# Optimization experiments

Measured on AMD Instinct MI355X. Metric: run time of the kernel, lower is better.

Reference implementation:

```python
import jax, jax.numpy as jnp
import numpy as np

DIM = 2048
N_HEADS = 32
N_KV_HEADS = 8
HEAD_DIM = DIM // N_HEADS  # 64
N_REP = N_HEADS // N_KV_HEADS  # 4
B, S = 2, 2048
MASK_VAL = -32768.0


def setup_inputs() -> dict:
    key = jax.random.key(0)
    ks = jax.random.split(key, 7)
    x = jax.random.normal(ks[0], (B, S, DIM), dtype=jnp.float32)
    freqs_cos = jax.random.uniform(ks[1], (S, HEAD_DIM // 2), dtype=jnp.float32)
    freqs_sin = jax.random.uniform(ks[2], (S, HEAD_DIM // 2), dtype=jnp.float32)
    sc = 1.0 / np.sqrt(DIM)
    wq = jax.random.normal(ks[3], (N_HEADS * HEAD_DIM, DIM), dtype=jnp.float32) * sc
    wk = jax.random.normal(ks[4], (N_KV_HEADS * HEAD_DIM, DIM), dtype=jnp.float32) * sc
    wv = jax.random.normal(ks[5], (N_KV_HEADS * HEAD_DIM, DIM), dtype=jnp.float32) * sc
    wo = jax.random.normal(ks[6], (DIM, N_HEADS * HEAD_DIM), dtype=jnp.float32) * sc
    return {"x": x, "freqs_cos": freqs_cos, "freqs_sin": freqs_sin,
            "wq": wq, "wk": wk, "wv": wv, "wo": wo}


def _apply_rope(q, k, cos, sin):
    # q: [B,S,H,D], k: [B,S,Hkv,D]; interleaved real/imag pairs in last dim
    def rot(t):
        tr = t.reshape(t.shape[:-1] + (-1, 2))  # [..., D/2, 2]
        t_r, t_i = tr[..., 0], tr[..., 1]
        c = cos[None, :, None, :]  # broadcast over batch and heads
        s = sin[None, :, None, :]
        o_r = t_r * c - t_i * s
        o_i = t_r * s + t_i * c
        return jnp.stack([o_r, o_i], axis=-1).reshape(t.shape)
    return rot(q), rot(k)


def reference(x, freqs_cos, freqs_sin, wq, wk, wv, wo):
    bsz, seqlen, _ = x.shape
    xq = (x @ wq.T).reshape(bsz, seqlen, N_HEADS, HEAD_DIM)
    xk = (x @ wk.T).reshape(bsz, seqlen, N_KV_HEADS, HEAD_DIM)
    xv = (x @ wv.T).reshape(bsz, seqlen, N_KV_HEADS, HEAD_DIM)
    xq, xk = _apply_rope(xq, xk, freqs_cos, freqs_sin)
    # GQA: repeat each kv head n_rep times contiguously (matches per-head cat loop)
    xk = jnp.repeat(xk, N_REP, axis=2)  # [B,S,H,D]
    xv = jnp.repeat(xv, N_REP, axis=2)
    # [B,H,S,D]
    q = xq.transpose(0, 2, 1, 3)
    k = xk.transpose(0, 2, 1, 3)
    v = xv.transpose(0, 2, 1, 3)
    scores = jnp.einsum('bhqd,bhkd->bhqk', q, k) / jnp.sqrt(jnp.float32(HEAD_DIM))
    causal = jnp.triu(jnp.full((seqlen, seqlen), MASK_VAL, dtype=scores.dtype), k=1)
    scores = scores + causal[None, None, :, :]
    probs = jax.nn.softmax(scores.astype(jnp.float32), axis=-1).astype(q.dtype)
    out = jnp.einsum('bhqk,bhkd->bhqd', probs, v)
    out = out.transpose(0, 2, 1, 3).reshape(bsz, seqlen, -1)
    return out @ wo.T
```

## Files before the change

### kernel.cpp

```cpp
#include <hip/hip_runtime.h>
#include <hip/hip_bf16.h>
#include <type_traits>

typedef __bf16 bf16;
typedef __bf16 bf16x2 __attribute__((ext_vector_type(2)));
typedef __bf16 bf16x4 __attribute__((ext_vector_type(4)));
typedef __bf16 bf16x8 __attribute__((ext_vector_type(8)));
typedef float f32x4 __attribute__((ext_vector_type(4)));

#define AS1 __attribute__((address_space(1)))
#define AS3 __attribute__((address_space(3)))

#define KAPPA 0.180336880111f

__device__ __forceinline__ void load_lds16(const void* g, void* l) {
  __builtin_amdgcn_global_load_lds((AS1 void*)g, (AS3 void*)l, 16, 0, 0);
}
__device__ __forceinline__ float exp2_fast(float x) {
  return __builtin_amdgcn_exp2f(x);
}

__global__ void f2b_all(const float* __restrict__ x, const float* __restrict__ wq,
                        const float* __restrict__ wk, const float* __restrict__ wv,
                        const float* __restrict__ wo, bf16* __restrict__ xb,
                        bf16* __restrict__ wqkv, bf16* __restrict__ wob) {
  int bid = blockIdx.x;
  if (bid < 8192) {
    int i = (bid * 256 + threadIdx.x) * 4;
    float4 v = *(const float4*)(x + i);
    bf16x4 o = {(bf16)v.x, (bf16)v.y, (bf16)v.z, (bf16)v.w};
    *(bf16x4*)(xb + i) = o;
    return;
  }
  int bid2 = bid - 8192;
  const float* src;
  bf16* dst;
  int nblk, kblk, nb;
  if (bid2 < 3072) {
    nblk = bid2 >> 6;
    kblk = bid2 & 63;
    int n0 = nblk * 64;
    if (n0 < 2048) { src = wq; nb = n0; }
    else if (n0 < 2560) { src = wk; nb = n0 - 2048; }
    else { src = wv; nb = n0 - 2560; }
    dst = wqkv;
  } else {
    int bid3 = bid2 - 3072;
    nblk = bid3 >> 6;
    kblk = bid3 & 63;
    src = wo;
    nb = nblk * 64;
    dst = wob;
  }
  const int t = threadIdx.x, j = t >> 6, l = t & 63;
  const int n = nb + j * 16 + (l & 15);
  const int k = kblk * 32 + (l >> 4) * 8;
  float4 v0 = *(const float4*)(src + (size_t)n * 2048 + k);
  float4 v1 = *(const float4*)(src + (size_t)n * 2048 + k + 4);
  bf16x8 o = {(bf16)v0.x, (bf16)v0.y, (bf16)v0.z, (bf16)v0.w,
              (bf16)v1.x, (bf16)v1.y, (bf16)v1.z, (bf16)v1.w};
  *(bf16x8*)((char*)dst + ((size_t)(nblk * 64 + kblk)) * 4096 + j * 1024 +
             l * 16) = o;
}

__global__ __launch_bounds__(256, 3) void gemm_qkv(const bf16* __restrict__ A,
                                                   const bf16* __restrict__ Bw,
                                                   const float* __restrict__ fc,
                                                   const float* __restrict__ fs,
                                                   bf16* __restrict__ Qro,
                                                   bf16* __restrict__ Kro,
                                                   bf16* __restrict__ Vt) {
  const int K = 2048;
  __shared__ bf16 As[3][128][32];
  const int t = threadIdx.x;
  const int wave = t >> 6, lane = t & 63, qd = lane >> 4, ln = lane & 15;
  const int wm = (wave >> 1) * 64;
  const int wn = (wave & 1) * 64;
  const int bn = blockIdx.x;
  const size_t bm = (size_t)blockIdx.y * 128;

  const bf16* Ab = A + bm * (size_t)K;
  const int n0 = bn * 2 + (wn >> 6);
  const char* Bb = (const char*)Bw + (size_t)n0 * 262144 + (size_t)lane * 16;

  auto stage = [&](int tk, int slot) {
#pragma unroll
    for (int sub = 0; sub < 2; sub++) {
      int e = sub * 256 + t;
      int ro = e >> 2, gs = (e & 3) ^ ((ro >> 1) & 3);
      load_lds16(Ab + (size_t)ro * K + tk * 32 + gs * 8,
                 (char*)As + slot * 8192 + sub * 4096 + wave * 1024);
    }
  };

  f32x4 acc[4][4] = {};
  const int segoff = (qd ^ ((ln >> 1) & 3)) << 4;
  bf16x8 b0[4], b1[4];

#pragma unroll
  for (int j = 0; j < 4; j++)
    b0[j] = *(const bf16x8*)(Bb + (size_t)j * 1024);
  stage(0, 0);
  stage(1, 1);
  asm volatile("s_waitcnt vmcnt(2)" ::: "memory");
  __builtin_amdgcn_s_barrier();

  auto step = [&](int tk, bf16x8 (&cb)[4], bf16x8 (&nb)[4]) {
    if (tk < 62) stage(tk + 2, (tk + 2) % 3);
    if (tk < 63) {
#pragma unroll
      for (int j = 0; j < 4; j++)
        nb[j] = *(const bf16x8*)(Bb + (size_t)(tk + 1) * 4096 + j * 1024);
    }
    const char* Asl = (const char*)As + (tk % 3) * 8192;
    bf16x8 af[4];
#pragma unroll
    for (int i = 0; i < 4; i++)
      af[i] = *(const bf16x8*)(Asl + (wm + i * 16 + ln) * 64 + segoff);
    if (tk <= 61) asm volatile("s_waitcnt lgkmcnt(0) vmcnt(6)" ::: "memory");
    else if (tk == 62) asm volatile("s_waitcnt lgkmcnt(0) vmcnt(4)" ::: "memory");
    else asm volatile("s_waitcnt lgkmcnt(0) vmcnt(0)" ::: "memory");
    __builtin_amdgcn_sched_barrier(0);
    __builtin_amdgcn_s_setprio(1);
#pragma unroll
    for (int i = 0; i < 4; i++)
#pragma unroll
      for (int j = 0; j < 4; j++)
        acc[i][j] = __builtin_amdgcn_mfma_f32_16x16x32_bf16(af[i], cb[j],
                                                            acc[i][j], 0, 0, 0);
    __builtin_amdgcn_s_setprio(0);
    if (tk < 63) __builtin_amdgcn_s_barrier();
  };

  for (int tk = 0; tk < 64; tk += 2) {
    step(tk, b0, b1);
    step(tk + 1, b1, b0);
  }

  const int b = (int)(bm >> 11);
  const int sb = (int)(bm & 2047) + wm;
  const bool odd = ln & 1;

  if (bn < 20) {
    const bool isQ = bn < 16;
    const float kap = isQ ? KAPPA : 1.0f;
    const int hh = isQ ? (bn * 2 + (wn >> 6)) : ((bn - 16) * 2 + (wn >> 6));
    bf16* dst = isQ ? (Qro + ((size_t)(b * 32 + hh) * 2048) * 64)
                    : (Kro + ((size_t)(b * 8 + hh) * 2048) * 64);
#pragma unroll
    for (int i = 0; i < 4; i++) {
#pragma unroll
      for (int j = 0; j < 4; j++) {
        const int d = j * 16 + ln;
        const int i_f = d >> 1;
#pragma unroll
        for (int r = 0; r < 4; r++) {
          int s = sb + i * 16 + qd * 4 + r;
          float v = acc[i][j][r];
          float p = __shfl_xor(v, 1);
          float cv = fc[s * 32 + i_f] * kap;
          float sv = fs[s * 32 + i_f] * kap;
          float o = odd ? (p * sv + v * cv) : (v * cv - p * sv);
          dst[(size_t)s * 64 + d] = (bf16)o;
        }
      }
    }
  } else {
    const int kh = (bn - 20) * 2 + (wn >> 6);
#pragma unroll
    for (int i = 0; i < 4; i++)
#pragma unroll
      for (int j = 0; j < 4; j++) {
        const int d = j * 16 + ln;
        int s = sb + i * 16 + qd * 4;
        bf16x4 ov = {(bf16)acc[i][j][0], (bf16)acc[i][j][1],
                     (bf16)acc[i][j][2], (bf16)acc[i][j][3]};
        *(bf16x4*)&Vt[((size_t)(b * 8 + kh) * 64 + d) * 2048 + s] = ov;
      }
  }
}

__global__ __launch_bounds__(256, 4) void gemm_bt(const bf16* __restrict__ A,
                                                  const bf16* __restrict__ Bw,
                                                  float* __restrict__ C) {
  const int K = 2048, N = 2048;
  __shared__ bf16 As[3][64][32];
  const int t = threadIdx.x;
  const int wave = t >> 6, lane = t & 63, qd = lane >> 4, ln = lane & 15;
  const int wm = (wave >> 1) * 32;
  const int wn = (wave & 1) * 64;
  const size_t bm = (size_t)blockIdx.y * 64;
  const size_t bn = (size_t)blockIdx.x * 128;

  const bf16* Ab = A + bm * (size_t)K;
  const int n0 = (int)(bn >> 6) + (wn >> 6);
  const char* Bb = (const char*)Bw + (size_t)n0 * 262144 + (size_t)lane * 16;

  auto stage = [&](int tk, int slot) {
    int ro = t >> 2, gs = (t & 3) ^ ((ro >> 1) & 3);
    load_lds16(Ab + (size_t)ro * K + tk * 32 + gs * 8,
               (char*)As + slot * 4096 + wave * 1024);
  };

  f32x4 acc[2][4] = {};
  const int segoff = (qd ^ ((ln >> 1) & 3)) << 4;
  bf16x8 b0[4], b1[4];

#pragma unroll
  for (int j = 0; j < 4; j++)
    b0[j] = *(const bf16x8*)(Bb + (size_t)j * 1024);
  stage(0, 0);
  stage(1, 1);
  asm volatile("s_waitcnt vmcnt(1)" ::: "memory");
  __builtin_amdgcn_s_barrier();

  auto step = [&](int tk, bf16x8 (&cb)[4], bf16x8 (&nb)[4]) {
    if (tk < 62) stage(tk + 2, (tk + 2) % 3);
    if (tk < 63) {
#pragma unroll
      for (int j = 0; j < 4; j++)
        nb[j] = *(const bf16x8*)(Bb + (size_t)(tk + 1) * 4096 + j * 1024);
    }
    const char* Asl = (const char*)As + (tk % 3) * 4096;
    bf16x8 af[2];
#pragma unroll
    for (int i = 0; i < 2; i++)
      af[i] = *(const bf16x8*)(Asl + (wm + i * 16 + ln) * 64 + segoff);
    if (tk <= 61) asm volatile("s_waitcnt lgkmcnt(0) vmcnt(5)" ::: "memory");
    else if (tk == 62) asm volatile("s_waitcnt lgkmcnt(0) vmcnt(4)" ::: "memory");
    else asm volatile("s_waitcnt lgkmcnt(0) vmcnt(0)" ::: "memory");
    __builtin_amdgcn_sched_barrier(0);
    __builtin_amdgcn_s_setprio(1);
#pragma unroll
    for (int i = 0; i < 2; i++)
#pragma unroll
      for (int j = 0; j < 4; j++)
        acc[i][j] = __builtin_amdgcn_mfma_f32_16x16x32_bf16(af[i], cb[j],
                                                            acc[i][j], 0, 0, 0);
    __builtin_amdgcn_s_setprio(0);
    if (tk < 63) __builtin_amdgcn_s_barrier();
  };

  for (int tk = 0; tk < 64; tk += 2) {
    step(tk, b0, b1);
    step(tk + 1, b1, b0);
  }

#pragma unroll
  for (int i = 0; i < 2; i++)
#pragma unroll
    for (int j = 0; j < 4; j++)
#pragma unroll
      for (int r = 0; r < 4; r++) {
        size_t row = bm + wm + i * 16 + qd * 4 + r;
        size_t col = bn + wn + j * 16 + ln;
        C[row * N + col] = acc[i][j][r];
      }
}

__global__ __launch_bounds__(256, 3) void attn_fwd(const bf16* __restrict__ Q,
                                                   const bf16* __restrict__ Kg,
                                                   const bf16* __restrict__ Vg,
                                                   bf16* __restrict__ O) {
  __shared__ bf16 Ks[2][64][64];
  __shared__ bf16 Vs[2][64][64];
  __shared__ bf16 Ps[128][64];
  const int t = threadIdx.x;
  const int wave = t >> 6, lane = t & 63, qd = lane >> 4, ln = lane & 15;
  const int bid = blockIdx.x;
  const int qt = 15 - (bid >> 6);
  const int bh = bid & 63;
  const int b = bh >> 5, h = bh & 31, kh = h >> 2;
  const bf16* Qb = Q + ((size_t)(b * 32 + h) * 2048 + qt * 128) * 64;
  const bf16* Kb = Kg + (size_t)(b * 8 + kh) * 2048 * 64;
  const bf16* Vb = Vg + (size_t)(b * 8 + kh) * 64 * 2048;
  char* PsB = (char*)Ps;

  bf16x8 qf[2][2];
#pragma unroll
  for (int kk = 0; kk < 2; kk++)
#pragma unroll
    for (int mi = 0; mi < 2; mi++)
      qf[kk][mi] = *(const bf16x8*)(Qb + (wave * 32 + mi * 16 + ln) * 64 +
                                    (kk * 4 + qd) * 8);

  auto stageKV = [&](int kb, int buf) {
#pragma unroll
    for (int i = 0; i < 2; i++) {
      int e = i * 256 + t;
      int row = e >> 3, sg = (e & 7) ^ (row & 7);
      load_lds16(Kb + (size_t)(kb * 64 + row) * 64 + sg * 8,
                 (char*)Ks + buf * 8192 + i * 4096 + wave * 1024);
      load_lds16(Vb + (size_t)row * 2048 + kb * 64 + sg * 8,
                 (char*)Vs + buf * 8192 + i * 4096 + wave * 1024);
    }
  };

  f32x4 o_acc[4][2] = {};
  float l_st[2] = {0.f, 0.f};
  const int q0 = qt * 128 + wave * 32;
  const int nkb = 2 * qt + 2;

  stageKV(0, 0);
  __syncthreads();

  for (int kb = 0; kb < nkb; kb++) {
    const int cur = kb & 1;
    if (kb + 1 < nkb) stageKV(kb + 1, cur ^ 1);
    const char* Ksl = (const char*)Ks + cur * 8192;
    const char* Vsl = (const char*)Vs + cur * 8192;

    f32x4 s_acc[4][2] = {};
#pragma unroll
    for (int kk = 0; kk < 2; kk++) {
      bf16x8 ak[4];
#pragma unroll
      for (int j = 0; j < 4; j++) {
        int row = j * 16 + ln;
        int ph = (kk * 4 + qd) ^ (ln & 7);
        ak[j] = *(const bf16x8*)(Ksl + row * 128 + ph * 16);
      }
#pragma unroll
      for (int j = 0; j < 4; j++)
#pragma unroll
        for (int mi = 0; mi < 2; mi++)
          s_acc[j][mi] = __builtin_amdgcn_mfma_f32_16x16x32_bf16(
              ak[j], qf[kk][mi], s_acc[j][mi], 0, 0, 0);
    }

    auto smax = [&](auto maskc) {
      constexpr bool MASK = decltype(maskc)::value;
#pragma unroll
      for (int mi = 0; mi < 2; mi++) {
        const int qv = q0 + mi * 16 + ln;
        const int prow = wave * 32 + mi * 16 + ln;
        float rs = 0.f;
#pragma unroll
        for (int j = 0; j < 4; j++) {
          bf16x4 pk;
#pragma unroll
          for (int r = 0; r < 4; r++) {
            float s = s_acc[j][mi][r];
            if (MASK) {
              int k_glob = kb * 64 + j * 16 + qd * 4 + r;
              if (k_glob > qv) s = -1e5f;
            }
            float pv = exp2_fast(s - 16.f);
            rs += pv;
            pk[r] = (bf16)pv;
          }
          int ps = (j * 2 + (qd >> 1)) ^ (ln & 7);
          *(bf16x4*)(PsB + prow * 128 + ps * 16 + (qd & 1) * 8) = pk;
        }
        l_st[mi] += rs;
      }
    };
    if (kb * 64 + 63 > q0) smax(std::true_type{});
    else smax(std::false_type{});

#pragma unroll
    for (int kk = 0; kk < 2; kk++) {
      bf16x8 av[4], bp[2];
#pragma unroll
      for (int dj = 0; dj < 4; dj++) {
        int row = dj * 16 + ln;
        int ph = (kk * 4 + qd) ^ (ln & 7);
        av[dj] = *(const bf16x8*)(Vsl + row * 128 + ph * 16);
      }
#pragma unroll
      for (int mi = 0; mi < 2; mi++) {
        int prow = wave * 32 + mi * 16 + ln;
        int ph = (kk * 4 + qd) ^ (ln & 7);
        bp[mi] = *(const bf16x8*)(PsB + prow * 128 + ph * 16);
      }
#pragma unroll
      for (int dj = 0; dj < 4; dj++)
#pragma unroll
        for (int mi = 0; mi < 2; mi++)
          o_acc[dj][mi] = __builtin_amdgcn_mfma_f32_16x16x32_bf16(
              av[dj], bp[mi], o_acc[dj][mi], 0, 0, 0);
    }

    __syncthreads();
  }

#pragma unroll
  for (int mi = 0; mi < 2; mi++) {
    float lt = l_st[mi];
    lt += __shfl_xor(lt, 16);
    lt += __shfl_xor(lt, 32);
    float inv = 1.f / lt;
    int q_idx = qt * 128 + wave * 32 + mi * 16 + ln;
#pragma unroll
    for (int dj = 0; dj < 4; dj++) {
      bf16x4 ov;
#pragma unroll
      for (int r = 0; r < 4; r++) ov[r] = (bf16)(o_acc[dj][mi][r] * inv);
      *(bf16x4*)&O[((size_t)(b * 2048 + q_idx) * 32 + h) * 64 + dj * 16 + qd * 4] = ov;
    }
  }
}

extern "C" void kernel_launch(void* const* d_in, const int* in_sizes, int n_in,
                              void* d_out, int out_size, void* d_ws,
                              size_t ws_size, hipStream_t stream) {
  const float* x = (const float*)d_in[0];
  const float* fc = (const float*)d_in[1];
  const float* fs = (const float*)d_in[2];
  const float* wq = (const float*)d_in[3];
  const float* wk = (const float*)d_in[4];
  const float* wv = (const float*)d_in[5];
  const float* wo = (const float*)d_in[6];
  float* out = (float*)d_out;

  char* ws = (char*)d_ws;
  const size_t MB = (size_t)1 << 20;
  bf16* xb   = (bf16*)(ws + 0 * MB);
  bf16* wqkv = (bf16*)(ws + 16 * MB);
  bf16* wob  = (bf16*)(ws + 28 * MB);
  bf16* Qro  = (bf16*)(ws + 36 * MB);
  bf16* Kro  = (bf16*)(ws + 52 * MB);
  bf16* Vt   = (bf16*)(ws + 56 * MB);
  bf16* Oa   = (bf16*)(ws + 60 * MB);

  dim3 blk(256);
  f2b_all<<<13312, blk, 0, stream>>>(x, wq, wk, wv, wo, xb, wqkv, wob);
  gemm_qkv<<<dim3(24, 32), blk, 0, stream>>>(xb, wqkv, fc, fs, Qro, Kro, Vt);
  attn_fwd<<<1024, blk, 0, stream>>>(Qro, Kro, Vt, Oa);
  gemm_bt<<<dim3(16, 64), blk, 0, stream>>>(Oa, wob, out);
}
```

Measured before the change: 281.5 us.

## Pre-swizzle activations into MFMA fragment layout and drop LDS staging in QKV GEMM

The fp32-to-bf16 conversion of x now writes the same blocked fragment layout already used for the weights, and the count of conversion blocks changes to match. The QKV GEMM then loads both A and B fragments directly from global memory into registers with a two-deep register double buffer. This removes LDS staging, barriers and manual waitcnt control. Each wave now fetches its own A tiles, so neighbouring waves no longer share them through LDS, which means more global and L2 traffic and less explicit latency hiding.

```diff
diff --git a/kernel.cpp b/kernel.cpp
--- a/kernel.cpp
+++ b/kernel.cpp
@@ -25,29 +25,28 @@
                         const float* __restrict__ wo, bf16* __restrict__ xb,
                         bf16* __restrict__ wqkv, bf16* __restrict__ wob) {
   int bid = blockIdx.x;
-  if (bid < 8192) {
-    int i = (bid * 256 + threadIdx.x) * 4;
-    float4 v = *(const float4*)(x + i);
-    bf16x4 o = {(bf16)v.x, (bf16)v.y, (bf16)v.z, (bf16)v.w};
-    *(bf16x4*)(xb + i) = o;
-    return;
-  }
-  int bid2 = bid - 8192;
   const float* src;
   bf16* dst;
   int nblk, kblk, nb;
-  if (bid2 < 3072) {
-    nblk = bid2 >> 6;
-    kblk = bid2 & 63;
+  if (bid < 4096) {
+    nblk = bid >> 6;
+    kblk = bid & 63;
+    src = x;
+    nb = nblk * 64;
+    dst = xb;
+  } else if (bid < 7168) {
+    int b2 = bid - 4096;
+    nblk = b2 >> 6;
+    kblk = b2 & 63;
     int n0 = nblk * 64;
     if (n0 < 2048) { src = wq; nb = n0; }
     else if (n0 < 2560) { src = wk; nb = n0 - 2048; }
     else { src = wv; nb = n0 - 2560; }
     dst = wqkv;
   } else {
-    int bid3 = bid2 - 3072;
-    nblk = bid3 >> 6;
-    kblk = bid3 & 63;
+    int b3 = bid - 7168;
+    nblk = b3 >> 6;
+    kblk = b3 & 63;
     src = wo;
     nb = nblk * 64;
     dst = wob;
@@ -70,8 +69,6 @@
                                                    bf16* __restrict__ Qro,
                                                    bf16* __restrict__ Kro,
                                                    bf16* __restrict__ Vt) {
-  const int K = 2048;
-  __shared__ bf16 As[3][128][32];
   const int t = threadIdx.x;
   const int wave = t >> 6, lane = t & 63, qd = lane >> 4, ln = lane & 15;
   const int wm = (wave >> 1) * 64;
@@ -79,62 +76,42 @@
   const int bn = blockIdx.x;
   const size_t bm = (size_t)blockIdx.y * 128;
 
-  const bf16* Ab = A + bm * (size_t)K;
+  const int mblk0 = (int)(blockIdx.y * 2) + (wm >> 6);
+  const char* Aw = (const char*)A + (size_t)mblk0 * 262144 + (size_t)lane * 16;
   const int n0 = bn * 2 + (wn >> 6);
   const char* Bb = (const char*)Bw + (size_t)n0 * 262144 + (size_t)lane * 16;
 
-  auto stage = [&](int tk, int slot) {
-#pragma unroll
-    for (int sub = 0; sub < 2; sub++) {
-      int e = sub * 256 + t;
-      int ro = e >> 2, gs = (e & 3) ^ ((ro >> 1) & 3);
-      load_lds16(Ab + (size_t)ro * K + tk * 32 + gs * 8,
-                 (char*)As + slot * 8192 + sub * 4096 + wave * 1024);
-    }
+  f32x4 acc[4][4] = {};
+  bf16x8 a0[4], b0[4], a1[4], b1[4];
+
+  auto loadT = [&](int tk, bf16x8 (&a)[4], bf16x8 (&b)[4]) {
+#pragma unroll
+    for (int i = 0; i < 4; i++)
+      a[i] = *(const bf16x8*)(Aw + (size_t)tk * 4096 + i * 1024);
+#pragma unroll
+    for (int j = 0; j < 4; j++)
+      b[j] = *(const bf16x8*)(Bb + (size_t)tk * 4096 + j * 1024);
   };
 
-  f32x4 acc[4][4] = {};
-  const int segoff = (qd ^ ((ln >> 1) & 3)) << 4;
-  bf16x8 b0[4], b1[4];
-
-#pragma unroll
-  for (int j = 0; j < 4; j++)
-    b0[j] = *(const bf16x8*)(Bb + (size_t)j * 1024);
-  stage(0, 0);
-  stage(1, 1);
-  asm volatile("s_waitcnt vmcnt(2)" ::: "memory");
-  __builtin_amdgcn_s_barrier();
-
-  auto step = [&](int tk, bf16x8 (&cb)[4], bf16x8 (&nb)[4]) {
-    if (tk < 62) stage(tk + 2, (tk + 2) % 3);
-    if (tk < 63) {
+  loadT(0, a0, b0);
+  loadT(1, a1, b1);
+
+  auto step = [&](int tk, bf16x8 (&ca)[4], bf16x8 (&cb)[4]) {
+    __builtin_amdgcn_s_setprio(1);
+#pragma unroll
+    for (int i = 0; i < 4; i++)
 #pragma unroll
       for (int j = 0; j < 4; j++)
-        nb[j] = *(const bf16x8*)(Bb + (size_t)(tk + 1) * 4096 + j * 1024);
-    }
-    const char* Asl = (const char*)As + (tk % 3) * 8192;
-    bf16x8 af[4];
-#pragma unroll
-    for (int i = 0; i < 4; i++)
-      af[i] = *(const bf16x8*)(Asl + (wm + i * 16 + ln) * 64 + segoff);
-    if (tk <= 61) asm volatile("s_waitcnt lgkmcnt(0) vmcnt(6)" ::: "memory");
-    else if (tk == 62) asm volatile("s_waitcnt lgkmcnt(0) vmcnt(4)" ::: "memory");
-    else asm volatile("s_waitcnt lgkmcnt(0) vmcnt(0)" ::: "memory");
-    __builtin_amdgcn_sched_barrier(0);
-    __builtin_amdgcn_s_setprio(1);
-#pragma unroll
-    for (int i = 0; i < 4; i++)
-#pragma unroll
-      for (int j = 0; j < 4; j++)
-        acc[i][j] = __builtin_amdgcn_mfma_f32_16x16x32_bf16(af[i], cb[j],
+        acc[i][j] = __builtin_amdgcn_mfma_f32_16x16x32_bf16(ca[i], cb[j],
                                                             acc[i][j], 0, 0, 0);
     __builtin_amdgcn_s_setprio(0);
-    if (tk < 63) __builtin_amdgcn_s_barrier();
+    if (tk + 2 < 64) loadT(tk + 2, ca, cb);
   };
 
+#pragma unroll 1
   for (int tk = 0; tk < 64; tk += 2) {
-    step(tk, b0, b1);
-    step(tk + 1, b1, b0);
+    step(tk, a0, b0);
+    step(tk + 1, a1, b1);
   }
 
   const int b = (int)(bm >> 11);
@@ -424,7 +401,7 @@
   bf16* Oa   = (bf16*)(ws + 60 * MB);
 
   dim3 blk(256);
-  f2b_all<<<13312, blk, 0, stream>>>(x, wq, wk, wv, wo, xb, wqkv, wob);
+  f2b_all<<<9216, blk, 0, stream>>>(x, wq, wk, wv, wo, xb, wqkv, wob);
   gemm_qkv<<<dim3(24, 32), blk, 0, stream>>>(xb, wqkv, fc, fs, Qro, Kro, Vt);
   attn_fwd<<<1024, blk, 0, stream>>>(Qro, Kro, Vt, Oa);
   gemm_bt<<<dim3(16, 64), blk, 0, stream>>>(Oa, wob, out);
```

New measurement: 288.4 us. 2.5% more time.
